# Optimization experiments

Measured on AMD Instinct MI355X. Metric: run time of the kernel, lower is better.

Reference implementation:

```python
import jax, jax.numpy as jnp
import numpy as np

N = 50000      # nodes
E = 800000     # edges (avg in-degree 16)
IN_DIM = 128
OUT_DIM = 64
LEAKY_SLOPE = 0.01  # torch F.leaky_relu default


def setup_inputs() -> dict:
    key = jax.random.key(0)
    ks = jax.random.split(key, 7)
    h = jax.random.normal(ks[0], (N, IN_DIM), dtype=jnp.float32)
    r_h = jax.random.normal(ks[1], (E, OUT_DIM), dtype=jnp.float32)
    edge_src = jax.random.randint(ks[2], (E,), 0, N, dtype=jnp.int32)
    edge_dst = jax.random.randint(ks[3], (E,), 0, N, dtype=jnp.int32)
    # learned params (xavier-ish scaling)
    W_fc = jax.random.normal(ks[4], (OUT_DIM, IN_DIM), dtype=jnp.float32) * (1.0 / np.sqrt(IN_DIM))
    attn_w = jax.random.normal(ks[5], (1, 3 * OUT_DIM), dtype=jnp.float32) * 0.1
    loop_weight = jax.random.normal(ks[6], (OUT_DIM, OUT_DIM), dtype=jnp.float32) * (1.0 / np.sqrt(OUT_DIM))
    return {"h": h, "r_h": r_h, "W_fc": W_fc, "attn_w": attn_w,
            "loop_weight": loop_weight, "edge_src": edge_src, "edge_dst": edge_dst}


def reference(h, r_h, W_fc, attn_w, loop_weight, edge_src, edge_dst):
    # z = fc(h)   [N, OUT_DIM]
    z = h @ W_fc.T
    z_src = z[edge_src]          # [E, OUT_DIM]
    z_dst = z[edge_dst]          # [E, OUT_DIM]
    # attn_fc(cat([z_src, z_dst, r_h])) expressed without materializing the concat
    w1 = attn_w[0, :OUT_DIM]
    w2 = attn_w[0, OUT_DIM:2 * OUT_DIM]
    w3 = attn_w[0, 2 * OUT_DIM:]
    a = z_src @ w1 + z_dst @ w2 + r_h @ w3            # [E]
    e = jax.nn.leaky_relu(a, LEAKY_SLOPE)
    # segment softmax over incoming edges of each destination node
    seg_max = jax.ops.segment_max(e, edge_dst, num_segments=N)  # -inf for deg-0 (never gathered)
    e_exp = jnp.exp(e - jax.lax.stop_gradient(seg_max)[edge_dst])
    denom = jax.ops.segment_sum(e_exp, edge_dst, num_segments=N)
    alpha = e_exp / denom[edge_dst]                   # [E]
    # weighted scatter-sum of source features
    agg = jax.ops.segment_sum(alpha[:, None] * z_src, edge_dst, num_segments=N)  # [N, OUT_DIM]
    # DGL only runs reduce_func (incl. self-loop matmul) on nodes with in-edges
    deg = jax.ops.segment_sum(jnp.ones((E,), jnp.float32), edge_dst, num_segments=N)
    h_out = jnp.where(deg[:, None] > 0, agg + z @ loop_weight, 0.0)
    return jax.nn.relu(h_out)
```

## Files before the change

### kernel.cpp

```cpp
#include <hip/hip_runtime.h>
#include <hip/hip_bf16.h>

#define NN 50000
#define EE 800000
#define IND 128
#define OUTD 64
#define NB 49
#define PA_BLOCKS 782
#define DEG_BLOCKS 391

__global__ __launch_bounds__(256) void k_front(
    const float* __restrict__ h, const float* __restrict__ W,
    const float* __restrict__ attn, const int* __restrict__ edst,
    float* __restrict__ z, __hip_bfloat16* __restrict__ zb,
    float* __restrict__ s1, float* __restrict__ s2,
    int* __restrict__ deg, int* __restrict__ rank) {
  if (blockIdx.x >= PA_BLOCKS) {
    const int base = (blockIdx.x - PA_BLOCKS) * 2048 + threadIdx.x;
#pragma unroll
    for (int j = 0; j < 8; ++j) {
      int e = base + j * 256;
      if (e < EE) rank[e] = atomicAdd(&deg[edst[e]], 1);
    }
    return;
  }
  __shared__ float Wl[64 * 129];
  const int tid = threadIdx.x;
#pragma unroll
  for (int j = 0; j < 8; ++j) {
    int i4 = tid + j * 256;
    const float4 v = reinterpret_cast<const float4*>(W)[i4];
    int i = i4 * 4;
    int col = i >> 7, k = i & 127;
    float* p = &Wl[col * 129 + k];
    p[0] = v.x; p[1] = v.y; p[2] = v.z; p[3] = v.w;
  }
  __syncthreads();
  const int lane = tid & 63;
  const int wid = tid >> 6;
  float Wreg[128];
#pragma unroll
  for (int k = 0; k < 128; ++k) Wreg[k] = Wl[lane * 129 + k];
  const float w1v = attn[lane];
  const float w2v = attn[64 + lane];
  const int base = blockIdx.x * 64 + wid * 16;
  for (int i = 0; i < 16; ++i) {
    int r = base + i;
    if (r >= NN) return;
    const float* hr = h + (size_t)r * IND;
    float h0 = hr[lane];
    float h1 = hr[64 + lane];
    float acc = 0.f;
#pragma unroll
    for (int k = 0; k < 64; ++k)
      acc = fmaf(__uint_as_float(__builtin_amdgcn_readlane(__float_as_uint(h0), k)),
                 Wreg[k], acc);
#pragma unroll
    for (int k = 0; k < 64; ++k)
      acc = fmaf(__uint_as_float(__builtin_amdgcn_readlane(__float_as_uint(h1), k)),
                 Wreg[64 + k], acc);
    z[(size_t)r * OUTD + lane] = acc;
    zb[(size_t)r * OUTD + lane] = __float2bfloat16(acc);
    float p = acc * w1v, q = acc * w2v;
#pragma unroll
    for (int m = 32; m >= 1; m >>= 1) {
      p += __shfl_xor(p, m, 64);
      q += __shfl_xor(q, m, 64);
    }
    if (lane == 0) { s1[r] = p; s2[r] = q; }
  }
}

__global__ __launch_bounds__(1024) void k_scan1(
    const int* __restrict__ deg, int* __restrict__ offL,
    int* __restrict__ blocksum) {
  __shared__ int wsum[16];
  __shared__ int woff[17];
  const int tid = threadIdx.x;
  const int gid = blockIdx.x * 1024 + tid;
  const int lane = tid & 63, wid = tid >> 6;
  int v = (gid < NN) ? deg[gid] : 0;
  int incl = v;
#pragma unroll
  for (int o = 1; o < 64; o <<= 1) {
    int t = __shfl_up(incl, o, 64);
    if (lane >= o) incl += t;
  }
  if (lane == 63) wsum[wid] = incl;
  __syncthreads();
  if (wid == 0 && lane < 16) {
    int s = wsum[lane];
    int si = s;
#pragma unroll
    for (int o = 1; o < 16; o <<= 1) {
      int t = __shfl_up(si, o, 64);
      if (lane >= o) si += t;
    }
    woff[lane] = si - s;
    if (lane == 15) woff[16] = si;
  }
  __syncthreads();
  if (gid < NN) offL[gid] = woff[wid] + incl - v;
  if (tid == 0) blocksum[blockIdx.x] = woff[16];
}

__global__ __launch_bounds__(64) void k_scan2(
    const int* __restrict__ blocksum, int* __restrict__ blockoff) {
  const int lane = threadIdx.x;
  int v = (lane < NB) ? blocksum[lane] : 0;
  int incl = v;
#pragma unroll
  for (int o = 1; o < 64; o <<= 1) {
    int t = __shfl_up(incl, o, 64);
    if (lane >= o) incl += t;
  }
  if (lane < NB) blockoff[lane] = incl - v;
}

__global__ __launch_bounds__(256) void k_attn_scatter(
    const float* __restrict__ r_h, const float* __restrict__ attn,
    const int* __restrict__ esrc, const int* __restrict__ edst,
    const float* __restrict__ s1, const float* __restrict__ s2,
    const int* __restrict__ rank, const int* __restrict__ offL,
    const int* __restrict__ blockoff, int2* __restrict__ pairs) {
  const int t = blockIdx.x * 256 + threadIdx.x;
  const int sub = t & 15;
  float4 rv = reinterpret_cast<const float4*>(r_h)[t];
  float4 wv = reinterpret_cast<const float4*>(attn + 2 * OUTD)[sub];
  float d = rv.x * wv.x + rv.y * wv.y + rv.z * wv.z + rv.w * wv.w;
  d += __shfl_xor(d, 1, 64);
  d += __shfl_xor(d, 2, 64);
  d += __shfl_xor(d, 4, 64);
  d += __shfl_xor(d, 8, 64);
  if (sub == 0) {
    const int e = t >> 4;
    int s = esrc[e], dd = edst[e];
    float a = s1[s] + s2[dd] + d;
    float el = a > 0.f ? a : 0.01f * a;
    float ex = __expf(el);
    int pos = blockoff[dd >> 10] + offL[dd] + rank[e];
    pairs[pos] = make_int2(s, __float_as_int(ex));
  }
}

__global__ __launch_bounds__(256) void k_agg(
    const float* __restrict__ z, const __hip_bfloat16* __restrict__ zb,
    const int2* __restrict__ pairs,
    const int* __restrict__ offL, const int* __restrict__ blockoff,
    const int* __restrict__ deg, const float* __restrict__ LW,
    float* __restrict__ out) {
  const int lane = threadIdx.x & 63, wid = threadIdx.x >> 6;
  const int slot = lane >> 4, sub = lane & 15;
  float4 LWreg[16];
#pragma unroll
  for (int kl = 0; kl < 16; ++kl)
    LWreg[kl] = reinterpret_cast<const float4*>(LW)[(slot * 16 + kl) * 16 + sub];
  const int r = blockIdx.x * 4 + wid;
  const int cnt = deg[r];
  const int2* pp = pairs + (blockoff[r >> 10] + offL[r]);
  float4 acc = make_float4(0.f, 0.f, 0.f, 0.f);
  float wsum = 0.f;
  for (int i = 0; i < cnt; i += 16) {
    int2 p[4];
    float w[4];
#pragma unroll
    for (int j = 0; j < 4; ++j) {
      int e = i + j * 4 + slot;
      bool v = e < cnt;
      p[j] = pp[v ? e : 0];
      w[j] = v ? __int_as_float(p[j].y) : 0.f;
    }
#pragma unroll
    for (int j = 0; j < 4; ++j) {
      ushort4 uz = reinterpret_cast<const ushort4*>(zb)[(size_t)p[j].x * 16 + sub];
      float zx = __uint_as_float((unsigned)uz.x << 16);
      float zy = __uint_as_float((unsigned)uz.y << 16);
      float zz = __uint_as_float((unsigned)uz.z << 16);
      float zw = __uint_as_float((unsigned)uz.w << 16);
      acc.x = fmaf(w[j], zx, acc.x);
      acc.y = fmaf(w[j], zy, acc.y);
      acc.z = fmaf(w[j], zz, acc.z);
      acc.w = fmaf(w[j], zw, acc.w);
      wsum += w[j];
    }
  }
  float4 lacc = make_float4(0.f, 0.f, 0.f, 0.f);
#pragma unroll
  for (int j = 0; j < 4; ++j) {
    float4 zq = reinterpret_cast<const float4*>(z)[(size_t)r * 16 + slot * 4 + j];
    float zk[4] = {zq.x, zq.y, zq.z, zq.w};
#pragma unroll
    for (int c = 0; c < 4; ++c) {
      float4 lw = LWreg[4 * j + c];
      lacc.x = fmaf(zk[c], lw.x, lacc.x);
      lacc.y = fmaf(zk[c], lw.y, lacc.y);
      lacc.z = fmaf(zk[c], lw.z, lacc.z);
      lacc.w = fmaf(zk[c], lw.w, lacc.w);
    }
  }
  wsum += __shfl_xor(wsum, 16, 64);
  wsum += __shfl_xor(wsum, 32, 64);
  float inv = (cnt > 0) ? 1.f / wsum : 0.f;
  float4 t;
  t.x = fmaf(acc.x, inv, lacc.x);
  t.y = fmaf(acc.y, inv, lacc.y);
  t.z = fmaf(acc.z, inv, lacc.z);
  t.w = fmaf(acc.w, inv, lacc.w);
  t.x += __shfl_xor(t.x, 16, 64); t.x += __shfl_xor(t.x, 32, 64);
  t.y += __shfl_xor(t.y, 16, 64); t.y += __shfl_xor(t.y, 32, 64);
  t.z += __shfl_xor(t.z, 16, 64); t.z += __shfl_xor(t.z, 32, 64);
  t.w += __shfl_xor(t.w, 16, 64); t.w += __shfl_xor(t.w, 32, 64);
  if (slot == 0) {
    float4 res;
    res.x = (cnt > 0 && t.x > 0.f) ? t.x : 0.f;
    res.y = (cnt > 0 && t.y > 0.f) ? t.y : 0.f;
    res.z = (cnt > 0 && t.z > 0.f) ? t.z : 0.f;
    res.w = (cnt > 0 && t.w > 0.f) ? t.w : 0.f;
    reinterpret_cast<float4*>(out)[(size_t)r * 16 + sub] = res;
  }
}

extern "C" void kernel_launch(void* const* d_in, const int* in_sizes, int n_in,
                              void* d_out, int out_size, void* d_ws, size_t ws_size,
                              hipStream_t stream) {
  const float* h    = (const float*)d_in[0];
  const float* r_h  = (const float*)d_in[1];
  const float* W_fc = (const float*)d_in[2];
  const float* attn = (const float*)d_in[3];
  const float* LW   = (const float*)d_in[4];
  const int* esrc   = (const int*)d_in[5];
  const int* edst   = (const int*)d_in[6];
  float* out = (float*)d_out;

  char* ws = (char*)d_ws;
  float* z            = (float*)(ws);
  __hip_bfloat16* zb  = (__hip_bfloat16*)(ws + 12800000);
  int2*  pairs = (int2*)(ws + 19200000);
  int*   rank  = (int*)(ws + 25600000);
  float* s1    = (float*)(ws + 28800000);
  float* s2    = (float*)(ws + 29000000);
  int*   deg   = (int*)(ws + 29200000);
  int*   offL  = (int*)(ws + 29400000);
  int*   bsum  = (int*)(ws + 29600000);
  int*   boff  = (int*)(ws + 29601024);

  hipMemsetAsync(deg, 0, (size_t)NN * sizeof(int), stream);

  k_front<<<PA_BLOCKS + DEG_BLOCKS, 256, 0, stream>>>(
      h, W_fc, attn, edst, z, zb, s1, s2, deg, rank);
  k_scan1<<<NB, 1024, 0, stream>>>(deg, offL, bsum);
  k_scan2<<<1, 64, 0, stream>>>(bsum, boff);
  k_attn_scatter<<<EE * 16 / 256, 256, 0, stream>>>(
      r_h, attn, esrc, edst, s1, s2, rank, offL, boff, pairs);
  k_agg<<<NN / 4, 256, 0, stream>>>(z, zb, pairs, offL, boff, deg, LW, out);
}
```

Measured before the change: 431.2 us.

## Move r_h attention dot into front kernel and drop fp32 z buffer

The r_h·w3 edge dot product moves out of the scatter kernel into extra blocks of the front kernel, writing a per-edge d3 array. This lets that 200MB-scale streaming read overlap with the GEMM and degree counting, and the scatter becomes one thread per edge. The fp32 z buffer is removed and the self-loop matmul now reads bf16 z, which saves bandwidth but lowers precision on that term. The front GEMM also splits its reduction across four accumulators to break the FMA dependency chain.

```diff
diff --git a/kernel.cpp b/kernel.cpp
--- a/kernel.cpp
+++ b/kernel.cpp
@@ -8,15 +8,37 @@
 #define NB 49
 #define PA_BLOCKS 782
 #define DEG_BLOCKS 391
+#define RH_BLOCKS 25000
 
 __global__ __launch_bounds__(256) void k_front(
     const float* __restrict__ h, const float* __restrict__ W,
     const float* __restrict__ attn, const int* __restrict__ edst,
-    float* __restrict__ z, __hip_bfloat16* __restrict__ zb,
-    float* __restrict__ s1, float* __restrict__ s2,
-    int* __restrict__ deg, int* __restrict__ rank) {
+    const float* __restrict__ r_h,
+    __hip_bfloat16* __restrict__ zb, float* __restrict__ s1,
+    float* __restrict__ s2, int* __restrict__ deg, int* __restrict__ rank,
+    float* __restrict__ d3) {
+  const int tid = threadIdx.x;
+  if (blockIdx.x >= PA_BLOCKS + DEG_BLOCKS) {
+    const int base = (blockIdx.x - (PA_BLOCKS + DEG_BLOCKS)) * 512 + tid;
+    const int sub = tid & 15;
+    float4 rv0 = reinterpret_cast<const float4*>(r_h)[base];
+    float4 rv1 = reinterpret_cast<const float4*>(r_h)[base + 256];
+    float4 wv = reinterpret_cast<const float4*>(attn + 2 * OUTD)[sub];
+    float d0 = rv0.x * wv.x + rv0.y * wv.y + rv0.z * wv.z + rv0.w * wv.w;
+    float d1 = rv1.x * wv.x + rv1.y * wv.y + rv1.z * wv.z + rv1.w * wv.w;
+#pragma unroll
+    for (int m = 1; m <= 8; m <<= 1) {
+      d0 += __shfl_xor(d0, m, 64);
+      d1 += __shfl_xor(d1, m, 64);
+    }
+    if (sub == 0) {
+      d3[base >> 4] = d0;
+      d3[(base >> 4) + 16] = d1;
+    }
+    return;
+  }
   if (blockIdx.x >= PA_BLOCKS) {
-    const int base = (blockIdx.x - PA_BLOCKS) * 2048 + threadIdx.x;
+    const int base = (blockIdx.x - PA_BLOCKS) * 2048 + tid;
 #pragma unroll
     for (int j = 0; j < 8; ++j) {
       int e = base + j * 256;
@@ -25,7 +47,6 @@
     return;
   }
   __shared__ float Wl[64 * 129];
-  const int tid = threadIdx.x;
 #pragma unroll
   for (int j = 0; j < 8; ++j) {
     int i4 = tid + j * 256;
@@ -50,16 +71,22 @@
     const float* hr = h + (size_t)r * IND;
     float h0 = hr[lane];
     float h1 = hr[64 + lane];
-    float acc = 0.f;
-#pragma unroll
-    for (int k = 0; k < 64; ++k)
-      acc = fmaf(__uint_as_float(__builtin_amdgcn_readlane(__float_as_uint(h0), k)),
-                 Wreg[k], acc);
-#pragma unroll
-    for (int k = 0; k < 64; ++k)
-      acc = fmaf(__uint_as_float(__builtin_amdgcn_readlane(__float_as_uint(h1), k)),
-                 Wreg[64 + k], acc);
-    z[(size_t)r * OUTD + lane] = acc;
+    float a0 = 0.f, a1 = 0.f, a2 = 0.f, a3 = 0.f;
+#pragma unroll
+    for (int k = 0; k < 16; ++k) {
+      a0 = fmaf(__uint_as_float(__builtin_amdgcn_readlane(__float_as_uint(h0), 4 * k)),     Wreg[4 * k], a0);
+      a1 = fmaf(__uint_as_float(__builtin_amdgcn_readlane(__float_as_uint(h0), 4 * k + 1)), Wreg[4 * k + 1], a1);
+      a2 = fmaf(__uint_as_float(__builtin_amdgcn_readlane(__float_as_uint(h0), 4 * k + 2)), Wreg[4 * k + 2], a2);
+      a3 = fmaf(__uint_as_float(__builtin_amdgcn_readlane(__float_as_uint(h0), 4 * k + 3)), Wreg[4 * k + 3], a3);
+    }
+#pragma unroll
+    for (int k = 0; k < 16; ++k) {
+      a0 = fmaf(__uint_as_float(__builtin_amdgcn_readlane(__float_as_uint(h1), 4 * k)),     Wreg[64 + 4 * k], a0);
+      a1 = fmaf(__uint_as_float(__builtin_amdgcn_readlane(__float_as_uint(h1), 4 * k + 1)), Wreg[64 + 4 * k + 1], a1);
+      a2 = fmaf(__uint_as_float(__builtin_amdgcn_readlane(__float_as_uint(h1), 4 * k + 2)), Wreg[64 + 4 * k + 2], a2);
+      a3 = fmaf(__uint_as_float(__builtin_amdgcn_readlane(__float_as_uint(h1), 4 * k + 3)), Wreg[64 + 4 * k + 3], a3);
+    }
+    float acc = (a0 + a1) + (a2 + a3);
     zb[(size_t)r * OUTD + lane] = __float2bfloat16(acc);
     float p = acc * w1v, q = acc * w2v;
 #pragma unroll
@@ -117,35 +144,24 @@
   if (lane < NB) blockoff[lane] = incl - v;
 }
 
-__global__ __launch_bounds__(256) void k_attn_scatter(
-    const float* __restrict__ r_h, const float* __restrict__ attn,
+__global__ __launch_bounds__(256) void k_scatter(
     const int* __restrict__ esrc, const int* __restrict__ edst,
-    const float* __restrict__ s1, const float* __restrict__ s2,
-    const int* __restrict__ rank, const int* __restrict__ offL,
-    const int* __restrict__ blockoff, int2* __restrict__ pairs) {
-  const int t = blockIdx.x * 256 + threadIdx.x;
-  const int sub = t & 15;
-  float4 rv = reinterpret_cast<const float4*>(r_h)[t];
-  float4 wv = reinterpret_cast<const float4*>(attn + 2 * OUTD)[sub];
-  float d = rv.x * wv.x + rv.y * wv.y + rv.z * wv.z + rv.w * wv.w;
-  d += __shfl_xor(d, 1, 64);
-  d += __shfl_xor(d, 2, 64);
-  d += __shfl_xor(d, 4, 64);
-  d += __shfl_xor(d, 8, 64);
-  if (sub == 0) {
-    const int e = t >> 4;
-    int s = esrc[e], dd = edst[e];
-    float a = s1[s] + s2[dd] + d;
-    float el = a > 0.f ? a : 0.01f * a;
-    float ex = __expf(el);
-    int pos = blockoff[dd >> 10] + offL[dd] + rank[e];
-    pairs[pos] = make_int2(s, __float_as_int(ex));
-  }
+    const float* __restrict__ d3, const float* __restrict__ s1,
+    const float* __restrict__ s2, const int* __restrict__ rank,
+    const int* __restrict__ offL, const int* __restrict__ blockoff,
+    int2* __restrict__ pairs) {
+  const int e = blockIdx.x * 256 + threadIdx.x;
+  if (e >= EE) return;
+  int s = esrc[e], dd = edst[e];
+  float a = s1[s] + s2[dd] + d3[e];
+  float el = a > 0.f ? a : 0.01f * a;
+  float ex = __expf(el);
+  int pos = blockoff[dd >> 10] + offL[dd] + rank[e];
+  pairs[pos] = make_int2(s, __float_as_int(ex));
 }
 
 __global__ __launch_bounds__(256) void k_agg(
-    const float* __restrict__ z, const __hip_bfloat16* __restrict__ zb,
-    const int2* __restrict__ pairs,
+    const __hip_bfloat16* __restrict__ zb, const int2* __restrict__ pairs,
     const int* __restrict__ offL, const int* __restrict__ blockoff,
     const int* __restrict__ deg, const float* __restrict__ LW,
     float* __restrict__ out) {
@@ -173,22 +189,21 @@
 #pragma unroll
     for (int j = 0; j < 4; ++j) {
       ushort4 uz = reinterpret_cast<const ushort4*>(zb)[(size_t)p[j].x * 16 + sub];
-      float zx = __uint_as_float((unsigned)uz.x << 16);
-      float zy = __uint_as_float((unsigned)uz.y << 16);
-      float zz = __uint_as_float((unsigned)uz.z << 16);
-      float zw = __uint_as_float((unsigned)uz.w << 16);
-      acc.x = fmaf(w[j], zx, acc.x);
-      acc.y = fmaf(w[j], zy, acc.y);
-      acc.z = fmaf(w[j], zz, acc.z);
-      acc.w = fmaf(w[j], zw, acc.w);
+      acc.x = fmaf(w[j], __uint_as_float((unsigned)uz.x << 16), acc.x);
+      acc.y = fmaf(w[j], __uint_as_float((unsigned)uz.y << 16), acc.y);
+      acc.z = fmaf(w[j], __uint_as_float((unsigned)uz.z << 16), acc.z);
+      acc.w = fmaf(w[j], __uint_as_float((unsigned)uz.w << 16), acc.w);
       wsum += w[j];
     }
   }
   float4 lacc = make_float4(0.f, 0.f, 0.f, 0.f);
 #pragma unroll
   for (int j = 0; j < 4; ++j) {
-    float4 zq = reinterpret_cast<const float4*>(z)[(size_t)r * 16 + slot * 4 + j];
-    float zk[4] = {zq.x, zq.y, zq.z, zq.w};
+    ushort4 uz = reinterpret_cast<const ushort4*>(zb)[(size_t)r * 16 + slot * 4 + j];
+    float zk[4] = {__uint_as_float((unsigned)uz.x << 16),
+                   __uint_as_float((unsigned)uz.y << 16),
+                   __uint_as_float((unsigned)uz.z << 16),
+                   __uint_as_float((unsigned)uz.w << 16)};
 #pragma unroll
     for (int c = 0; c < 4; ++c) {
       float4 lw = LWreg[4 * j + c];
@@ -233,24 +248,24 @@
   float* out = (float*)d_out;
 
   char* ws = (char*)d_ws;
-  float* z            = (float*)(ws);
-  __hip_bfloat16* zb  = (__hip_bfloat16*)(ws + 12800000);
-  int2*  pairs = (int2*)(ws + 19200000);
-  int*   rank  = (int*)(ws + 25600000);
-  float* s1    = (float*)(ws + 28800000);
-  float* s2    = (float*)(ws + 29000000);
-  int*   deg   = (int*)(ws + 29200000);
-  int*   offL  = (int*)(ws + 29400000);
-  int*   bsum  = (int*)(ws + 29600000);
-  int*   boff  = (int*)(ws + 29601024);
+  __hip_bfloat16* zb = (__hip_bfloat16*)(ws);
+  int2*  pairs = (int2*)(ws + 6400000);
+  int*   rank  = (int*)(ws + 12800000);
+  float* d3    = (float*)(ws + 16000000);
+  float* s1    = (float*)(ws + 19200000);
+  float* s2    = (float*)(ws + 19400000);
+  int*   deg   = (int*)(ws + 19600000);
+  int*   offL  = (int*)(ws + 19800000);
+  int*   bsum  = (int*)(ws + 20000000);
+  int*   boff  = (int*)(ws + 20001024);
 
   hipMemsetAsync(deg, 0, (size_t)NN * sizeof(int), stream);
 
-  k_front<<<PA_BLOCKS + DEG_BLOCKS, 256, 0, stream>>>(
-      h, W_fc, attn, edst, z, zb, s1, s2, deg, rank);
+  k_front<<<PA_BLOCKS + DEG_BLOCKS + RH_BLOCKS, 256, 0, stream>>>(
+      h, W_fc, attn, edst, r_h, zb, s1, s2, deg, rank, d3);
   k_scan1<<<NB, 1024, 0, stream>>>(deg, offL, bsum);
   k_scan2<<<1, 64, 0, stream>>>(bsum, boff);
-  k_attn_scatter<<<EE * 16 / 256, 256, 0, stream>>>(
-      r_h, attn, esrc, edst, s1, s2, rank, offL, boff, pairs);
-  k_agg<<<NN / 4, 256, 0, stream>>>(z, zb, pairs, offL, boff, deg, LW, out);
-}
+  k_scatter<<<(EE + 255) / 256, 256, 0, stream>>>(
+      esrc, edst, d3, s1, s2, rank, offL, boff, pairs);
+  k_agg<<<NN / 4, 256, 0, stream>>>(zb, pairs, offL, boff, deg, LW, out);
+}
```

After: 422.8 us. Within noise of the previous version (-1.9%).
